# Kernel tuning notes

Hardware: AMD Instinct MI355X
Metric: run time of the kernel (lower is better)

Reference implementation:

```python
import jax, jax.numpy as jnp
import numpy as np

D_MODEL = 768
N_HEADS = 12
D_K = D_MODEL // N_HEADS


def setup_inputs() -> dict:
    key = jax.random.key(0)
    kq, kk, kv, kwq, kbq, kwo, kbo = jax.random.split(key, 7)
    B, S = 1, 4096
    s = 1.0 / np.sqrt(D_MODEL)
    return {
        "q": jax.random.normal(kq, (B, S, D_MODEL), jnp.float32),
        "k": jax.random.normal(kk, (B, S, D_MODEL), jnp.float32),
        "v": jax.random.normal(kv, (B, S, D_MODEL), jnp.float32),
        # nn.Linear weights stored as [out, in]; note the original forward
        # uses W_q for Q, K, AND V (W_k/W_v are never used), so only W_q and
        # W_o are materialized here.
        "Wq": jax.random.uniform(kwq, (D_MODEL, D_MODEL), jnp.float32, -s, s),
        "bq": jax.random.uniform(kbq, (D_MODEL,), jnp.float32, -s, s),
        "Wo": jax.random.uniform(kwo, (D_MODEL, D_MODEL), jnp.float32, -s, s),
        "bo": jax.random.uniform(kbo, (D_MODEL,), jnp.float32, -s, s),
    }


def _split_heads(x):  # [B,S,D] -> [B,H,S,Dk]
    B, S, _ = x.shape
    return x.reshape(B, S, N_HEADS, D_K).transpose(0, 2, 1, 3)


def reference(q, k, v, Wq, bq, Wo, bo):
    # Faithful to source: same W_q projection applied to q, k, v.
    Q = _split_heads(q @ Wq.T + bq)
    K = _split_heads(k @ Wq.T + bq)
    V = _split_heads(v @ Wq.T + bq)
    scale = 1.0 / np.sqrt(D_K).astype(np.float32)
    scores = jnp.einsum("bhqd,bhkd->bhqk", Q, K) * scale  # [B,H,S,S]
    probs = jax.nn.softmax(scores, axis=-1)
    atten = jnp.einsum("bhqk,bhkd->bhqd", probs, V)
    B, _, S, _ = atten.shape
    concat = atten.transpose(0, 2, 1, 3).reshape(B, S, D_MODEL)
    return concat @ Wo.T + bo
```

## Files before the change

### kernel.cpp

```cpp
#include <hip/hip_runtime.h>
#include <stdint.h>
#include <math.h>


#define SQ 4096
#define DM 768
#define NH 12

typedef float f32x4 __attribute__((ext_vector_type(4)));
typedef short bf16x8 __attribute__((ext_vector_type(8)));
typedef unsigned int u32x4 __attribute__((ext_vector_type(4)));
typedef unsigned short ushort_t;

static __device__ __forceinline__ ushort_t f2bf(float f) {
    unsigned int u = __builtin_bit_cast(unsigned int, f);
    u += 0x7fffu + ((u >> 16) & 1u);
    return (ushort_t)(u >> 16);
}

static __device__ __forceinline__ unsigned int cvt_pk_bf16(float a, float b) {
    unsigned int d;
    asm("v_cvt_pk_bf16_f32 %0, %1, %2" : "=v"(d) : "v"(a), "v"(b));
    return d;
}

static __device__ __forceinline__ float exp2_hw(float x) {
    float r;
    asm("v_exp_f32 %0, %1" : "=v"(r) : "v"(x));
    return r;
}

static __device__ __forceinline__ void gload16(const ushort_t* g, ushort_t* l) {
    __builtin_amdgcn_global_load_lds(
        reinterpret_cast<const __attribute__((address_space(1))) unsigned int*>(
            reinterpret_cast<uintptr_t>(g)),
        reinterpret_cast<__attribute__((address_space(3))) unsigned int*>(
            reinterpret_cast<uintptr_t>(l)),
        16, 0, 0);
}

__global__ __launch_bounds__(256) void cvt_all(
    const float* __restrict__ q, const float* __restrict__ k,
    const float* __restrict__ v, const float* __restrict__ Wq,
    const float* __restrict__ Wo, ushort_t* __restrict__ xb,
    ushort_t* __restrict__ wqb, ushort_t* __restrict__ wob) {
    const int NE4 = (SQ * DM) / 4;
    const int NW4 = (DM * DM) / 4;
    int i = blockIdx.x * 256 + threadIdx.x;
    const float* src;
    ushort_t* dst;
    if (i < NE4) { src = q; dst = xb; }
    else if (i < 2 * NE4) { src = k; dst = xb + SQ * DM; i -= NE4; }
    else if (i < 3 * NE4) { src = v; dst = xb + 2 * SQ * DM; i -= 2 * NE4; }
    else if (i < 3 * NE4 + NW4) { src = Wq; dst = wqb; i -= 3 * NE4; }
    else if (i < 3 * NE4 + 2 * NW4) { src = Wo; dst = wob; i -= 3 * NE4 + NW4; }
    else return;
    float4 x = reinterpret_cast<const float4*>(src)[i];
    ushort4 o;
    o.x = f2bf(x.x); o.y = f2bf(x.y); o.z = f2bf(x.z); o.w = f2bf(x.w);
    reinterpret_cast<ushort4*>(dst)[i] = o;
}

template <int EPI>
__global__ __launch_bounds__(256) void gemm_bf16(
    const ushort_t* __restrict__ A, const ushort_t* __restrict__ B,
    const float* __restrict__ bias, ushort_t* __restrict__ proj,
    ushort_t* __restrict__ vt, float* __restrict__ outf) {
    __shared__ __align__(16) ushort_t lsA[128 * 64];
    __shared__ __align__(16) ushort_t lsB[128 * 64];
    const int tid = threadIdx.x;
    const int lane = tid & 63;
    const int w = tid >> 6;
    const int wm = w >> 1, wn = w & 1;
    const int g = lane >> 4, li = lane & 15;
    const int bm = blockIdx.x / 6, bn = blockIdx.x % 6;
    const int arow = bm * 128, brow = bn * 128;
    const int sr = lane >> 3;
    const int sc = ((lane & 7) ^ sr) * 8;

    f32x4 acc[4][4] = {};

    for (int kt = 0; kt < 12; ++kt) {
        const int k0 = kt * 64;
        __syncthreads();
#pragma unroll
        for (int c = 0; c < 4; ++c) {
            const int chunk = w * 4 + c;
            const int r = chunk * 8 + sr;
            gload16(A + (size_t)(arow + r) * DM + k0 + sc, lsA + chunk * 512);
            gload16(B + (size_t)(brow + r) * DM + k0 + sc, lsB + chunk * 512);
        }
        __syncthreads();

        bf16x8 af[4][2];
#pragma unroll
        for (int mf = 0; mf < 4; ++mf) {
            const int row = wm * 64 + mf * 16 + li;
#pragma unroll
            for (int ks = 0; ks < 2; ++ks)
                af[mf][ks] = *reinterpret_cast<const bf16x8*>(
                    lsA + row * 64 + ((ks * 32 + g * 8) ^ ((li & 7) << 3)));
        }
#pragma unroll
        for (int nf = 0; nf < 4; ++nf) {
            const int row = wn * 64 + nf * 16 + li;
            bf16x8 b0 = *reinterpret_cast<const bf16x8*>(
                lsB + row * 64 + ((g * 8) ^ ((li & 7) << 3)));
            bf16x8 b1 = *reinterpret_cast<const bf16x8*>(
                lsB + row * 64 + ((32 + g * 8) ^ ((li & 7) << 3)));
#pragma unroll
            for (int mf = 0; mf < 4; ++mf) {
                acc[mf][nf] = __builtin_amdgcn_mfma_f32_16x16x32_bf16(af[mf][0], b0, acc[mf][nf], 0, 0, 0);
                acc[mf][nf] = __builtin_amdgcn_mfma_f32_16x16x32_bf16(af[mf][1], b1, acc[mf][nf], 0, 0, 0);
            }
        }
    }

    if (EPI == 0) {
        const bool isV = (arow >= 8192);
        const float qscale = (arow < 4096) ? 0.18033688011112042f : 1.0f;
#pragma unroll
        for (int nf = 0; nf < 4; ++nf) {
            const int col = brow + wn * 64 + nf * 16 + li;
            const float bv = bias[col];
#pragma unroll
            for (int mf = 0; mf < 4; ++mf) {
                const int row0 = arow + wm * 64 + mf * 16 + g * 4;
                if (!isV) {
#pragma unroll
                    for (int r = 0; r < 4; ++r)
                        proj[(size_t)(row0 + r) * DM + col] = f2bf((acc[mf][nf][r] + bv) * qscale);
                } else {
                    ushort4 pk;
                    pk.x = f2bf(acc[mf][nf][0] + bv);
                    pk.y = f2bf(acc[mf][nf][1] + bv);
                    pk.z = f2bf(acc[mf][nf][2] + bv);
                    pk.w = f2bf(acc[mf][nf][3] + bv);
                    const int kv = row0 - 8192;
                    const int pos = (kv & ~31) | ((kv & 0xC) << 1) | (((kv >> 4) & 1) << 2);
                    *reinterpret_cast<ushort4*>(vt + (size_t)col * SQ + pos) = pk;
                }
            }
        }
    } else {
#pragma unroll
        for (int nf = 0; nf < 4; ++nf) {
            const int col = brow + wn * 64 + nf * 16 + li;
            const float bv = bias[col];
#pragma unroll
            for (int mf = 0; mf < 4; ++mf) {
                const int row0 = arow + wm * 64 + mf * 16 + g * 4;
#pragma unroll
                for (int r = 0; r < 4; ++r)
                    outf[(size_t)(row0 + r) * DM + col] = acc[mf][nf][r] + bv;
            }
        }
    }
}

__global__ __launch_bounds__(128) void attn_bf16(
    const ushort_t* __restrict__ qk, const ushort_t* __restrict__ vtb,
    ushort_t* __restrict__ cc) {
    __shared__ __align__(16) ushort_t kl[2][64 * 64];
    __shared__ __align__(16) ushort_t vl[2][64 * 64];

    const int tid = threadIdx.x, lane = tid & 63, w = tid >> 6;
    const int g = lane >> 4, li = lane & 15;
    const int logical = (blockIdx.x & 7) * 96 + (blockIdx.x >> 3);
    const int h = logical >> 6, qb = logical & 63;
    const int sr = lane >> 3;
    const int sc = ((lane & 7) ^ sr) * 8;

    const ushort_t* Kb = qk + (size_t)4096 * DM + (size_t)h * 64;
    const ushort_t* Vb = vtb + (size_t)(h * 64) * SQ;

    bf16x8 qf[2][2];
#pragma unroll
    for (int qh = 0; qh < 2; ++qh)
#pragma unroll
        for (int ks = 0; ks < 2; ++ks)
            qf[qh][ks] = *reinterpret_cast<const bf16x8*>(
                qk + (size_t)(qb * 64 + w * 32 + qh * 16 + li) * DM + h * 64 + ks * 32 + g * 8);

    f32x4 oacc[2][4] = {};
    float lsum0 = 0.f, lsum1 = 0.f;

#pragma unroll
    for (int c = 0; c < 4; ++c) {
        const int ch = w * 4 + c;
        const int r = ch * 8 + sr;
        gload16(Kb + (size_t)r * DM + sc, &kl[0][ch * 512]);
        gload16(Vb + (size_t)r * SQ + sc, &vl[0][ch * 512]);
    }
    __syncthreads();

#define STEP(kp, vp, kn, vn, kvn)                                              \
    do {                                                                       \
        if ((kvn) < 64) {                                                      \
            const int kvo = (kvn) * 64;                                        \
            _Pragma("unroll") for (int c = 0; c < 4; ++c) {                    \
                const int ch = w * 4 + c;                                      \
                const int r = ch * 8 + sr;                                     \
                gload16(Kb + (size_t)(kvo + r) * DM + sc, &(kn)[ch * 512]);    \
                gload16(Vb + (size_t)r * SQ + kvo + sc, &(vn)[ch * 512]);      \
            }                                                                  \
        }                                                                      \
        f32x4 sf[2][4] = {};                                                   \
        __builtin_amdgcn_s_setprio(1);                                         \
        _Pragma("unroll") for (int nf = 0; nf < 4; ++nf) {                     \
            const int row = nf * 16 + li;                                      \
            bf16x8 kb0 = *reinterpret_cast<const bf16x8*>(                     \
                (kp) + row * 64 + ((g * 8) ^ ((li & 7) << 3)));                \
            bf16x8 kb1 = *reinterpret_cast<const bf16x8*>(                     \
                (kp) + row * 64 + ((32 + g * 8) ^ ((li & 7) << 3)));           \
            _Pragma("unroll") for (int qh = 0; qh < 2; ++qh) {                 \
                sf[qh][nf] = __builtin_amdgcn_mfma_f32_16x16x32_bf16(          \
                    kb0, qf[qh][0], sf[qh][nf], 0, 0, 0);                      \
                sf[qh][nf] = __builtin_amdgcn_mfma_f32_16x16x32_bf16(          \
                    kb1, qf[qh][1], sf[qh][nf], 0, 0, 0);                      \
            }                                                                  \
        }                                                                      \
        __builtin_amdgcn_s_setprio(0);                                         \
        _Pragma("unroll") for (int qh = 0; qh < 2; ++qh)                       \
            _Pragma("unroll") for (int nf = 0; nf < 4; ++nf) {                 \
                f32x4 p;                                                       \
                _Pragma("unroll") for (int r = 0; r < 4; ++r)                  \
                    p[r] = exp2_hw(sf[qh][nf][r]);                             \
                sf[qh][nf] = p;                                                \
                const float ps = (p[0] + p[1]) + (p[2] + p[3]);                \
                if (qh == 0) lsum0 += ps; else lsum1 += ps;                    \
            }                                                                  \
        __builtin_amdgcn_s_setprio(1);                                         \
        _Pragma("unroll") for (int ks = 0; ks < 2; ++ks) {                     \
            bf16x8 pa[2];                                                      \
            _Pragma("unroll") for (int qh = 0; qh < 2; ++qh) {                 \
                u32x4 pu;                                                      \
                pu.x = cvt_pk_bf16(sf[qh][2 * ks][0], sf[qh][2 * ks][1]);      \
                pu.y = cvt_pk_bf16(sf[qh][2 * ks][2], sf[qh][2 * ks][3]);      \
                pu.z = cvt_pk_bf16(sf[qh][2 * ks + 1][0], sf[qh][2 * ks + 1][1]); \
                pu.w = cvt_pk_bf16(sf[qh][2 * ks + 1][2], sf[qh][2 * ks + 1][3]); \
                pa[qh] = __builtin_bit_cast(bf16x8, pu);                       \
            }                                                                  \
            _Pragma("unroll") for (int nv = 0; nv < 4; ++nv) {                 \
                const int vrow = nv * 16 + li;                                 \
                bf16x8 vb = *reinterpret_cast<const bf16x8*>(                  \
                    (vp) + vrow * 64 + ((ks * 32 + g * 8) ^ ((li & 7) << 3))); \
                oacc[0][nv] = __builtin_amdgcn_mfma_f32_16x16x32_bf16(         \
                    pa[0], vb, oacc[0][nv], 0, 0, 0);                          \
                oacc[1][nv] = __builtin_amdgcn_mfma_f32_16x16x32_bf16(         \
                    pa[1], vb, oacc[1][nv], 0, 0, 0);                          \
            }                                                                  \
        }                                                                      \
        __builtin_amdgcn_s_setprio(0);                                         \
        __syncthreads();                                                       \
    } while (0)

#pragma unroll 1
    for (int t = 0; t < 32; ++t) {
        STEP(&kl[0][0], &vl[0][0], &kl[1][0], &vl[1][0], 2 * t + 1);
        STEP(&kl[1][0], &vl[1][0], &kl[0][0], &vl[0][0], 2 * t + 2);
    }
#undef STEP

#pragma unroll
    for (int qh = 0; qh < 2; ++qh) {
        float s = (qh == 0) ? lsum0 : lsum1;
        s += __shfl_xor(s, 16);
        s += __shfl_xor(s, 32);
        float inv[4];
        const int gbase = g << 2;
#pragma unroll
        for (int r = 0; r < 4; ++r)
            inv[r] = 1.0f / __shfl(s, gbase + r);
#pragma unroll
        for (int nv = 0; nv < 4; ++nv)
#pragma unroll
            for (int r = 0; r < 4; ++r) {
                const int row = qb * 64 + w * 32 + qh * 16 + g * 4 + r;
                const int col = h * 64 + nv * 16 + li;
                cc[(size_t)row * DM + col] = f2bf(oacc[qh][nv][r] * inv[r]);
            }
    }
}

extern "C" void kernel_launch(void* const* d_in, const int* in_sizes, int n_in,
                              void* d_out, int out_size, void* d_ws, size_t ws_size,
                              hipStream_t stream) {
    const float* q = (const float*)d_in[0];
    const float* k = (const float*)d_in[1];
    const float* v = (const float*)d_in[2];
    const float* Wq = (const float*)d_in[3];
    const float* bq = (const float*)d_in[4];
    const float* Wo = (const float*)d_in[5];
    const float* bo = (const float*)d_in[6];
    float* out = (float*)d_out;

    ushort_t* ws = (ushort_t*)d_ws;
    const int NE = SQ * DM;
    ushort_t* xb = ws;
    ushort_t* wqb = ws + 3 * NE;
    ushort_t* wob = wqb + DM * DM;
    ushort_t* proj = wob + DM * DM;
    ushort_t* vt = proj + 2 * NE;
    ushort_t* cc = vt + NE;

    const int n4 = 3 * (NE / 4) + 2 * ((DM * DM) / 4);
    cvt_all<<<(n4 + 255) / 256, 256, 0, stream>>>(q, k, v, Wq, Wo, xb, wqb, wob);

    gemm_bf16<0><<<(12288 / 128) * 6, 256, 0, stream>>>(xb, wqb, bq, proj, vt, (float*)nullptr);

    attn_bf16<<<NH * (SQ / 64), 128, 0, stream>>>(proj, vt, cc);

    gemm_bf16<1><<<(SQ / 128) * 6, 256, 0, stream>>>(cc, wob, bo, (ushort_t*)nullptr, (ushort_t*)nullptr, out);
}
```

Baseline: 147.1 us.

## Split attention KV range across two wave pairs per block and reduce in LDS

The attention kernel now launches 256 threads per block. Two wave pairs each process half of the key/value sequence, with 32-key tiles per step instead of 64, and the partial output accumulators and row sums are combined through shared memory at the end. This doubles the waves per workgroup so more latency can be hidden, at the cost of an extra LDS reduction, a final barrier, and smaller per-step tiles. Because softmax uses no running max, the partial sums add directly without rescaling.

New measurement: 137.4 us. 1.07x faster.

```diff
diff --git a/kernel.cpp b/kernel.cpp
--- a/kernel.cpp
+++ b/kernel.cpp
@@ -158,21 +158,24 @@
     }
 }
 
-__global__ __launch_bounds__(128) void attn_bf16(
+__global__ __launch_bounds__(256) void attn_bf16(
     const ushort_t* __restrict__ qk, const ushort_t* __restrict__ vtb,
     ushort_t* __restrict__ cc) {
-    __shared__ __align__(16) ushort_t kl[2][64 * 64];
-    __shared__ __align__(16) ushort_t vl[2][64 * 64];
+    __shared__ __align__(16) ushort_t kl[2][2][32 * 64];
+    __shared__ __align__(16) ushort_t vl[2][2][64 * 32];
 
     const int tid = threadIdx.x, lane = tid & 63, w = tid >> 6;
+    const int wp = w & 1, p = w >> 1;
     const int g = lane >> 4, li = lane & 15;
     const int logical = (blockIdx.x & 7) * 96 + (blockIdx.x >> 3);
     const int h = logical >> 6, qb = logical & 63;
     const int sr = lane >> 3;
     const int sc = ((lane & 7) ^ sr) * 8;
-
-    const ushort_t* Kb = qk + (size_t)4096 * DM + (size_t)h * 64;
-    const ushort_t* Vb = vtb + (size_t)(h * 64) * SQ;
+    const int vdr = lane >> 2;
+    const int vsc = ((lane & 3) ^ (vdr & 3)) * 8;
+
+    const ushort_t* Kb = qk + (size_t)(4096 + p * 2048) * DM + (size_t)h * 64;
+    const ushort_t* Vb = vtb + (size_t)(h * 64) * SQ + p * 2048;
 
     bf16x8 qf[2][2];
 #pragma unroll
@@ -180,34 +183,34 @@
 #pragma unroll
         for (int ks = 0; ks < 2; ++ks)
             qf[qh][ks] = *reinterpret_cast<const bf16x8*>(
-                qk + (size_t)(qb * 64 + w * 32 + qh * 16 + li) * DM + h * 64 + ks * 32 + g * 8);
+                qk + (size_t)(qb * 64 + wp * 32 + qh * 16 + li) * DM + h * 64 + ks * 32 + g * 8);
 
     f32x4 oacc[2][4] = {};
     float lsum0 = 0.f, lsum1 = 0.f;
 
 #pragma unroll
-    for (int c = 0; c < 4; ++c) {
-        const int ch = w * 4 + c;
-        const int r = ch * 8 + sr;
-        gload16(Kb + (size_t)r * DM + sc, &kl[0][ch * 512]);
-        gload16(Vb + (size_t)r * SQ + sc, &vl[0][ch * 512]);
+    for (int c = 0; c < 2; ++c) {
+        const int ch = wp * 2 + c;
+        gload16(Kb + (size_t)(ch * 8 + sr) * DM + sc, &kl[p][0][ch * 512]);
+        gload16(Vb + (size_t)(ch * 16 + vdr) * SQ + vsc, &vl[p][0][ch * 512]);
     }
     __syncthreads();
 
 #define STEP(kp, vp, kn, vn, kvn)                                              \
     do {                                                                       \
         if ((kvn) < 64) {                                                      \
-            const int kvo = (kvn) * 64;                                        \
-            _Pragma("unroll") for (int c = 0; c < 4; ++c) {                    \
-                const int ch = w * 4 + c;                                      \
-                const int r = ch * 8 + sr;                                     \
-                gload16(Kb + (size_t)(kvo + r) * DM + sc, &(kn)[ch * 512]);    \
-                gload16(Vb + (size_t)r * SQ + kvo + sc, &(vn)[ch * 512]);      \
+            const int kvo = (kvn) * 32;                                        \
+            _Pragma("unroll") for (int c = 0; c < 2; ++c) {                    \
+                const int ch = wp * 2 + c;                                     \
+                gload16(Kb + (size_t)(kvo + ch * 8 + sr) * DM + sc,            \
+                        &(kn)[ch * 512]);                                      \
+                gload16(Vb + (size_t)(ch * 16 + vdr) * SQ + kvo + vsc,         \
+                        &(vn)[ch * 512]);                                      \
             }                                                                  \
         }                                                                      \
-        f32x4 sf[2][4] = {};                                                   \
+        f32x4 sf[2][2] = {};                                                   \
         __builtin_amdgcn_s_setprio(1);                                         \
-        _Pragma("unroll") for (int nf = 0; nf < 4; ++nf) {                     \
+        _Pragma("unroll") for (int nf = 0; nf < 2; ++nf) {                     \
             const int row = nf * 16 + li;                                      \
             bf16x8 kb0 = *reinterpret_cast<const bf16x8*>(                     \
                 (kp) + row * 64 + ((g * 8) ^ ((li & 7) << 3)));                \
@@ -222,64 +225,94 @@
         }                                                                      \
         __builtin_amdgcn_s_setprio(0);                                         \
         _Pragma("unroll") for (int qh = 0; qh < 2; ++qh)                       \
-            _Pragma("unroll") for (int nf = 0; nf < 4; ++nf) {                 \
-                f32x4 p;                                                       \
+            _Pragma("unroll") for (int nf = 0; nf < 2; ++nf) {                 \
+                f32x4 pe;                                                      \
                 _Pragma("unroll") for (int r = 0; r < 4; ++r)                  \
-                    p[r] = exp2_hw(sf[qh][nf][r]);                             \
-                sf[qh][nf] = p;                                                \
-                const float ps = (p[0] + p[1]) + (p[2] + p[3]);                \
+                    pe[r] = exp2_hw(sf[qh][nf][r]);                            \
+                sf[qh][nf] = pe;                                               \
+                const float ps = (pe[0] + pe[1]) + (pe[2] + pe[3]);            \
                 if (qh == 0) lsum0 += ps; else lsum1 += ps;                    \
             }                                                                  \
         __builtin_amdgcn_s_setprio(1);                                         \
-        _Pragma("unroll") for (int ks = 0; ks < 2; ++ks) {                     \
-            bf16x8 pa[2];                                                      \
-            _Pragma("unroll") for (int qh = 0; qh < 2; ++qh) {                 \
-                u32x4 pu;                                                      \
-                pu.x = cvt_pk_bf16(sf[qh][2 * ks][0], sf[qh][2 * ks][1]);      \
-                pu.y = cvt_pk_bf16(sf[qh][2 * ks][2], sf[qh][2 * ks][3]);      \
-                pu.z = cvt_pk_bf16(sf[qh][2 * ks + 1][0], sf[qh][2 * ks + 1][1]); \
-                pu.w = cvt_pk_bf16(sf[qh][2 * ks + 1][2], sf[qh][2 * ks + 1][3]); \
-                pa[qh] = __builtin_bit_cast(bf16x8, pu);                       \
-            }                                                                  \
-            _Pragma("unroll") for (int nv = 0; nv < 4; ++nv) {                 \
-                const int vrow = nv * 16 + li;                                 \
-                bf16x8 vb = *reinterpret_cast<const bf16x8*>(                  \
-                    (vp) + vrow * 64 + ((ks * 32 + g * 8) ^ ((li & 7) << 3))); \
-                oacc[0][nv] = __builtin_amdgcn_mfma_f32_16x16x32_bf16(         \
-                    pa[0], vb, oacc[0][nv], 0, 0, 0);                          \
-                oacc[1][nv] = __builtin_amdgcn_mfma_f32_16x16x32_bf16(         \
-                    pa[1], vb, oacc[1][nv], 0, 0, 0);                          \
-            }                                                                  \
+        bf16x8 pa[2];                                                          \
+        _Pragma("unroll") for (int qh = 0; qh < 2; ++qh) {                     \
+            u32x4 pu;                                                          \
+            pu.x = cvt_pk_bf16(sf[qh][0][0], sf[qh][0][1]);                    \
+            pu.y = cvt_pk_bf16(sf[qh][0][2], sf[qh][0][3]);                    \
+            pu.z = cvt_pk_bf16(sf[qh][1][0], sf[qh][1][1]);                    \
+            pu.w = cvt_pk_bf16(sf[qh][1][2], sf[qh][1][3]);                    \
+            pa[qh] = __builtin_bit_cast(bf16x8, pu);                           \
+        }                                                                      \
+        _Pragma("unroll") for (int nv = 0; nv < 4; ++nv) {                     \
+            const int vrow = nv * 16 + li;                                     \
+            bf16x8 vb = *reinterpret_cast<const bf16x8*>(                      \
+                (vp) + vrow * 32 + ((g ^ (li & 3)) * 8));                      \
+            oacc[0][nv] = __builtin_amdgcn_mfma_f32_16x16x32_bf16(             \
+                pa[0], vb, oacc[0][nv], 0, 0, 0);                              \
+            oacc[1][nv] = __builtin_amdgcn_mfma_f32_16x16x32_bf16(             \
+                pa[1], vb, oacc[1][nv], 0, 0, 0);                              \
         }                                                                      \
         __builtin_amdgcn_s_setprio(0);                                         \
         __syncthreads();                                                       \
     } while (0)
 
+    {
+        ushort_t* k0p = &kl[p][0][0];
+        ushort_t* v0p = &vl[p][0][0];
+        ushort_t* k1p = &kl[p][1][0];
+        ushort_t* v1p = &vl[p][1][0];
 #pragma unroll 1
-    for (int t = 0; t < 32; ++t) {
-        STEP(&kl[0][0], &vl[0][0], &kl[1][0], &vl[1][0], 2 * t + 1);
-        STEP(&kl[1][0], &vl[1][0], &kl[0][0], &vl[0][0], 2 * t + 2);
+        for (int t = 0; t < 32; ++t) {
+            STEP(k0p, v0p, k1p, v1p, 2 * t + 1);
+            STEP(k1p, v1p, k0p, v0p, 2 * t + 2);
+        }
     }
 #undef STEP
 
-#pragma unroll
-    for (int qh = 0; qh < 2; ++qh) {
-        float s = (qh == 0) ? lsum0 : lsum1;
-        s += __shfl_xor(s, 16);
-        s += __shfl_xor(s, 32);
-        float inv[4];
-        const int gbase = g << 2;
-#pragma unroll
-        for (int r = 0; r < 4; ++r)
-            inv[r] = 1.0f / __shfl(s, gbase + r);
-#pragma unroll
-        for (int nv = 0; nv < 4; ++nv)
-#pragma unroll
-            for (int r = 0; r < 4; ++r) {
-                const int row = qb * 64 + w * 32 + qh * 16 + g * 4 + r;
-                const int col = h * 64 + nv * 16 + li;
-                cc[(size_t)row * DM + col] = f2bf(oacc[qh][nv][r] * inv[r]);
+    float* ob = reinterpret_cast<float*>(&kl[0][0][0]);
+    float* lsb = ob + 4096;
+    if (p == 1) {
+#pragma unroll
+        for (int qh = 0; qh < 2; ++qh) {
+#pragma unroll
+            for (int nv = 0; nv < 4; ++nv)
+                *reinterpret_cast<f32x4*>(
+                    ob + (((wp * 2 + qh) * 4 + nv) * 64 + lane) * 4) = oacc[qh][nv];
+            lsb[(wp * 2 + qh) * 64 + lane] = (qh == 0) ? lsum0 : lsum1;
+        }
+    }
+    __syncthreads();
+    if (p == 0) {
+        lsum0 += lsb[(wp * 2 + 0) * 64 + lane];
+        lsum1 += lsb[(wp * 2 + 1) * 64 + lane];
+#pragma unroll
+        for (int qh = 0; qh < 2; ++qh)
+#pragma unroll
+            for (int nv = 0; nv < 4; ++nv) {
+                f32x4 o = *reinterpret_cast<const f32x4*>(
+                    ob + (((wp * 2 + qh) * 4 + nv) * 64 + lane) * 4);
+                oacc[qh][nv] += o;
             }
+
+#pragma unroll
+        for (int qh = 0; qh < 2; ++qh) {
+            float s = (qh == 0) ? lsum0 : lsum1;
+            s += __shfl_xor(s, 16);
+            s += __shfl_xor(s, 32);
+            float inv[4];
+            const int gbase = g << 2;
+#pragma unroll
+            for (int r = 0; r < 4; ++r)
+                inv[r] = 1.0f / __shfl(s, gbase + r);
+#pragma unroll
+            for (int nv = 0; nv < 4; ++nv)
+#pragma unroll
+                for (int r = 0; r < 4; ++r) {
+                    const int row = qb * 64 + wp * 32 + qh * 16 + g * 4 + r;
+                    const int col = h * 64 + nv * 16 + li;
+                    cc[(size_t)row * DM + col] = f2bf(oacc[qh][nv][r] * inv[r]);
+                }
+        }
     }
 }
 
@@ -309,7 +342,7 @@
 
     gemm_bf16<0><<<(12288 / 128) * 6, 256, 0, stream>>>(xb, wqb, bq, proj, vt, (float*)nullptr);
 
-    attn_bf16<<<NH * (SQ / 64), 128, 0, stream>>>(proj, vt, cc);
+    attn_bf16<<<NH * (SQ / 64), 256, 0, stream>>>(proj, vt, cc);
 
     gemm_bf16<1><<<(SQ / 128) * 6, 256, 0, stream>>>(cc, wob, bo, (ushort_t*)nullptr, (ushort_t*)nullptr, out);
 }
```
